# Optimization experiments

Hardware: AMD Instinct MI355X
Metric: run time of the kernel (lower is better)

## Reference

```python
import jax, jax.numpy as jnp
import numpy as np

N, E, G, L, H, DIN = 50000, 800000, 500, 4, 64, 128
EPS = 1e-5


def _gcn(x, W, b, src, dst, n):
    h = x @ W
    loop = jnp.arange(n)
    s = jnp.concatenate([src, loop])
    d = jnp.concatenate([dst, loop])
    deg = jax.ops.segment_sum(jnp.ones(s.shape[0], x.dtype), d, num_segments=n)
    dinv = jax.lax.rsqrt(jnp.maximum(deg, 1.0))  # deg >= 1 due to self loops
    norm = (dinv[s] * dinv[d])[:, None]
    return jax.ops.segment_sum(h[s] * norm, d, num_segments=n) + b


def _g2(x, W, b, src, dst, n, p=2.0):
    # G2 gradient gate: tau = tanh(scatter_mean_over_src(|X_src - X_dst|^p))
    Xc = jax.nn.relu(_gcn(x, W, b, src, dst, n))
    diff = jnp.abs(Xc[src] - Xc[dst]) ** p  # [E, H]
    s = jax.ops.segment_sum(diff, src, num_segments=n)
    cnt = jax.ops.segment_sum(jnp.ones(src.shape[0], x.dtype), src, num_segments=n)
    return jnp.tanh(s / jnp.maximum(cnt, 1.0)[:, None])


def _bn(x, g, b):
    # BatchNorm1d with batch statistics (training-mode normalization)
    m = x.mean(0)
    v = x.var(0)
    return (x - m) * jax.lax.rsqrt(v + EPS) * g + b


def setup_inputs() -> dict:
    key = jax.random.key(0)
    ks = jax.random.split(key, 24)
    sc_in = 1.0 / np.sqrt(DIN)
    sc_h = 1.0 / np.sqrt(H)
    inp = {
        "x": jax.random.normal(ks[0], (N, DIN), jnp.float32),
        "edge_index": jax.random.randint(ks[1], (2, E), 0, N),
        "batch": jnp.sort(jax.random.randint(ks[2], (N,), 0, G)),
        "preW": jax.random.normal(ks[3], (DIN, H), jnp.float32) * sc_in,
        "preb": jnp.zeros((H,), jnp.float32),
        "convW": jax.random.normal(ks[4], (L, H, H), jnp.float32) * sc_h,
        "convb": jnp.zeros((L, H), jnp.float32),
        "ggW": jax.random.normal(ks[5], (L, H, H), jnp.float32) * sc_h,
        "ggb": jnp.zeros((L, H), jnp.float32),
        "lin1W": jax.random.normal(ks[6], (H, H), jnp.float32) * sc_h,
        "lin1b": jnp.zeros((H,), jnp.float32),
        "lin2W": jax.random.normal(ks[7], (H, H), jnp.float32) * sc_h,
        "lin2b": jnp.zeros((H,), jnp.float32),
        "lin3W": jax.random.normal(ks[8], (H, H), jnp.float32) * sc_h,
        "lin3b": jnp.zeros((H,), jnp.float32),
        "lin4W": jax.random.normal(ks[9], (H, 1), jnp.float32) * sc_h,
        "lin4b": jnp.zeros((1,), jnp.float32),
        "bn_g": jnp.ones((H,), jnp.float32),
        "bn_b": jnp.zeros((H,), jnp.float32),
    }
    return inp


def reference(x, edge_index, batch, preW, preb, convW, convb, ggW, ggb,
              lin1W, lin1b, lin2W, lin2b, lin3W, lin3b, lin4W, lin4b,
              bn_g, bn_b):
    src, dst = edge_index[0], edge_index[1]
    # prelinear (dropout disabled / eval)
    x = jax.nn.relu(x @ preW + preb)
    for l in range(L):
        x_ = jax.nn.relu(_gcn(x, convW[l], convb[l], src, dst, N))
        tau = _g2(x, ggW[l], ggb[l], src, dst, N)
        x = (1.0 - tau) * x + tau * x_
    # readout: global add pool per graph -> [G, H]
    h = jax.ops.segment_sum(x, batch, num_segments=G)
    out = jax.nn.relu(_bn(h @ lin1W + lin1b, bn_g, bn_b))
    out = jax.nn.relu(_bn(out @ lin2W + lin2b, bn_g, bn_b))
    out = jax.nn.relu(_bn(out @ lin3W + lin3b, bn_g, bn_b))
    out = out @ lin4W + lin4b  # [G, 1]
    energy = 0.5 * jnp.sum((x[src] - x[dst]) ** 2)  # dirichlet energy of final x
    return (out, out, energy)
```

## Files before the change

kernel.cpp:

```cpp
#include <hip/hip_runtime.h>
#include <hip/hip_bf16.h>


#define N_NODES 50000
#define N_EDGES 800000
#define N_GRAPH 500
#define N_LAYERS 4
#define HDIM 64
#define DDIN 128
#define BN_EPS 1e-5f
#define NEPART 256
#define SC_CHUNK 2048
#define SC_NBLK ((N_NODES + SC_CHUNK - 1) / SC_CHUNK)
#define NPARTS 8
#define PRNG (N_NODES / NPARTS)
#define FILL_BPP 56

typedef __hip_bfloat16 bf16;


__global__ __launch_bounds__(256) void k_degrees(const int* __restrict__ ei,
                                                 int* __restrict__ deg_in,
                                                 int* __restrict__ deg_out) {
  int part = blockIdx.x & (NPARTS - 1);
  int slice = blockIdx.x >> 3;
  int nslice = gridDim.x >> 3;
  int lo = part * PRNG, hi = lo + PRNG;
  int stride = nslice * 256;
  for (int e = slice * 256 + threadIdx.x; e < N_EDGES; e += stride) {
    int s = ei[e], d = ei[N_EDGES + e];
    if (s >= lo && s < hi) atomicAdd(&deg_out[s], 1);
    if (d >= lo && d < hi) atomicAdd(&deg_in[d], 1);
  }
}

__global__ __launch_bounds__(256) void k_scan1(const int* __restrict__ deg_in,
                                               const int* __restrict__ deg_out,
                                               int* __restrict__ rp_dst,
                                               int* __restrict__ rp_src,
                                               int* __restrict__ bsum) {
  int arr = blockIdx.y;
  const int* in = arr ? deg_out : deg_in;
  int* out = arr ? rp_src : rp_dst;
  int base = blockIdx.x * SC_CHUNK + threadIdx.x * 8;
  int v[8];
  int s = 0;
#pragma unroll
  for (int j = 0; j < 8; ++j) {
    int ii = base + j;
    v[j] = (ii < N_NODES) ? in[ii] : 0;
    s += v[j];
  }
  __shared__ int sh[256];
  sh[threadIdx.x] = s;
  __syncthreads();
  for (int off = 1; off < 256; off <<= 1) {
    int t = (threadIdx.x >= off) ? sh[threadIdx.x - off] : 0;
    __syncthreads();
    sh[threadIdx.x] += t;
    __syncthreads();
  }
  int run = sh[threadIdx.x] - s;
#pragma unroll
  for (int j = 0; j < 8; ++j) {
    int ii = base + j;
    if (ii < N_NODES) out[ii] = run;
    run += v[j];
  }
  if (threadIdx.x == 255) bsum[arr * SC_NBLK + blockIdx.x] = sh[255];
}

__global__ __launch_bounds__(64) void k_scan2(const int* __restrict__ bsum,
                                              int* __restrict__ boff,
                                              int* __restrict__ rp_dst,
                                              int* __restrict__ rp_src) {
  int lane = threadIdx.x;
  for (int a = 0; a < 2; ++a) {
    int v = (lane < SC_NBLK) ? bsum[a * SC_NBLK + lane] : 0;
    int incl = v;
    for (int off = 1; off < 64; off <<= 1) {
      int t = __shfl_up(incl, off);
      if (lane >= off) incl += t;
    }
    if (lane < SC_NBLK) boff[a * SC_NBLK + lane] = incl - v;
  }
  if (lane == 0) {
    rp_dst[N_NODES] = N_EDGES;
    rp_src[N_NODES] = N_EDGES;
  }
}

__global__ __launch_bounds__(256) void k_scan3(const int* __restrict__ boff,
                                               int* __restrict__ rp_dst,
                                               int* __restrict__ rp_src,
                                               int* __restrict__ cur_dst,
                                               int* __restrict__ cur_src,
                                               const int* __restrict__ deg_in,
                                               float* __restrict__ dinv) {
  int arr = blockIdx.y;
  int* rp = arr ? rp_src : rp_dst;
  int* cur = arr ? cur_src : cur_dst;
  int off = boff[arr * SC_NBLK + blockIdx.x];
  int base = blockIdx.x * SC_CHUNK + threadIdx.x * 8;
#pragma unroll
  for (int j = 0; j < 8; ++j) {
    int ii = base + j;
    if (ii < N_NODES) {
      int v = rp[ii] + off;
      rp[ii] = v;
      cur[ii] = v;
      if (arr == 0) dinv[ii] = rsqrtf((float)(deg_in[ii] + 1));
    }
  }
}

__global__ __launch_bounds__(256) void k_fill(const int* __restrict__ ei,
                                              int* __restrict__ cur_dst,
                                              int* __restrict__ cur_src,
                                              int* __restrict__ csr_dst,
                                              int* __restrict__ csr_src) {
  int part = blockIdx.x & (NPARTS - 1);
  int slice = blockIdx.x >> 3;
  int nslice = gridDim.x >> 3;
  int lo = part * PRNG, hi = lo + PRNG;
  int stride = nslice * 256;
  for (int e = slice * 256 + threadIdx.x; e < N_EDGES; e += stride) {
    int s = ei[e], d = ei[N_EDGES + e];
    if (d >= lo && d < hi) {
      int q = atomicAdd(&cur_dst[d], 1);
      csr_dst[q] = s;
    }
    if (s >= lo && s < hi) {
      int q = atomicAdd(&cur_src[s], 1);
      csr_src[q] = d;
    }
  }
}


__global__ __launch_bounds__(256) void k_prelin(const float* __restrict__ x0,
                                                const float* __restrict__ W,
                                                const float* __restrict__ b,
                                                const float* __restrict__ dinv,
                                                float* __restrict__ x,
                                                float* __restrict__ xs) {
  __shared__ float Ws[DDIN * HDIM];
  for (int t = threadIdx.x; t < DDIN * HDIM; t += 256) Ws[t] = W[t];
  __syncthreads();
  int wave = threadIdx.x >> 6, lane = threadIdx.x & 63;
  float bias = b[lane];
  int stride = gridDim.x * 4;
  for (int i = blockIdx.x * 4 + wave; i < N_NODES; i += stride) {
    const float* xr = x0 + (size_t)i * DDIN;
    float xl0 = xr[lane], xl1 = xr[64 + lane];
    float acc = bias;
#pragma unroll
    for (int k = 0; k < 64; ++k) acc = fmaf(__shfl(xl0, k), Ws[k * 64 + lane], acc);
#pragma unroll
    for (int k = 0; k < 64; ++k) acc = fmaf(__shfl(xl1, k), Ws[(64 + k) * 64 + lane], acc);
    float xv = fmaxf(acc, 0.f);
    size_t li = (size_t)i * HDIM + lane;
    x[li] = xv;
    xs[li] = xv * dinv[i];
  }
}

__global__ __launch_bounds__(256) void k_agg(const float* __restrict__ xs,
                                             const int* __restrict__ rp,
                                             const int* __restrict__ csr,
                                             const float* __restrict__ dinv,
                                             float* __restrict__ aggb) {
  int i = (blockIdx.x * 256 + threadIdx.x) >> 6;
  int lane = threadIdx.x & 63;
  if (i >= N_NODES) return;
  int e0 = rp[i], e1 = rp[i + 1];
  float di = dinv[i];
  size_t li = (size_t)i * HDIM + lane;
  float a0 = xs[li], a1 = 0.f, a2 = 0.f, a3 = 0.f;
  for (int base = e0; base < e1; base += 64) {
    int m = e1 - base;
    if (m > 64) m = 64;
    int idx = csr[base + (lane < m ? lane : 0)];
    int k = 0;
    for (; k + 8 <= m; k += 8) {
      int s0 = __shfl(idx, k), s1 = __shfl(idx, k + 1), s2 = __shfl(idx, k + 2),
          s3 = __shfl(idx, k + 3), s4 = __shfl(idx, k + 4), s5 = __shfl(idx, k + 5),
          s6 = __shfl(idx, k + 6), s7 = __shfl(idx, k + 7);
      float v0 = xs[(size_t)s0 * HDIM + lane], v1 = xs[(size_t)s1 * HDIM + lane];
      float v2 = xs[(size_t)s2 * HDIM + lane], v3 = xs[(size_t)s3 * HDIM + lane];
      float v4 = xs[(size_t)s4 * HDIM + lane], v5 = xs[(size_t)s5 * HDIM + lane];
      float v6 = xs[(size_t)s6 * HDIM + lane], v7 = xs[(size_t)s7 * HDIM + lane];
      a0 += v0;
      a1 += v1;
      a2 += v2;
      a3 += v3;
      a0 += v4;
      a1 += v5;
      a2 += v6;
      a3 += v7;
    }
    for (; k < m; ++k) {
      int s = __shfl(idx, k);
      a0 += xs[(size_t)s * HDIM + lane];
    }
  }
  aggb[li] = (a0 + a1 + a2 + a3) * di;
}

__global__ __launch_bounds__(256) void k_gemm2(const float* __restrict__ agg,
                                               const float* __restrict__ W1,
                                               const float* __restrict__ W2,
                                               const float* __restrict__ b1,
                                               const float* __restrict__ b2,
                                               float* __restrict__ x_,
                                               bf16* __restrict__ Xch) {
  __shared__ float W1s[HDIM * HDIM], W2s[HDIM * HDIM];
  for (int t = threadIdx.x; t < HDIM * HDIM; t += 256) {
    W1s[t] = W1[t];
    W2s[t] = W2[t];
  }
  __syncthreads();
  int wave = threadIdx.x >> 6, lane = threadIdx.x & 63;
  float bb1 = b1[lane], bb2 = b2[lane];
  int stride = gridDim.x * 4;
  for (int i = blockIdx.x * 4 + wave; i < N_NODES; i += stride) {
    size_t li = (size_t)i * HDIM + lane;
    float xl = agg[li];
    float r1 = 0.f, r2 = 0.f;
#pragma unroll
    for (int k = 0; k < 64; ++k) {
      float xv = __shfl(xl, k);
      r1 = fmaf(xv, W1s[k * 64 + lane], r1);
      r2 = fmaf(xv, W2s[k * 64 + lane], r2);
    }
    x_[li] = fmaxf(r1 + bb1, 0.f);
    Xch[li] = __float2bfloat16(fmaxf(r2 + bb2, 0.f));
  }
}

__global__ __launch_bounds__(256) void k_gate(const bf16* __restrict__ Xch,
                                              const float* __restrict__ x_,
                                              const int* __restrict__ rp,
                                              const int* __restrict__ csr,
                                              const float* __restrict__ dinv,
                                              float* __restrict__ x,
                                              bf16* __restrict__ xh,
                                              float* __restrict__ xs) {
  int i = (blockIdx.x * 256 + threadIdx.x) >> 6;
  int lane = threadIdx.x & 63;
  if (i >= N_NODES) return;
  int e0 = rp[i], e1 = rp[i + 1];
  float xi = __bfloat162float(Xch[(size_t)i * HDIM + lane]);
  float a0 = 0.f, a1 = 0.f, a2 = 0.f, a3 = 0.f;
  for (int base = e0; base < e1; base += 64) {
    int m = e1 - base;
    if (m > 64) m = 64;
    int idx = csr[base + (lane < m ? lane : 0)];
    int k = 0;
    for (; k + 8 <= m; k += 8) {
      int s0 = __shfl(idx, k), s1 = __shfl(idx, k + 1), s2 = __shfl(idx, k + 2),
          s3 = __shfl(idx, k + 3), s4 = __shfl(idx, k + 4), s5 = __shfl(idx, k + 5),
          s6 = __shfl(idx, k + 6), s7 = __shfl(idx, k + 7);
      float v0 = __bfloat162float(Xch[(size_t)s0 * HDIM + lane]);
      float v1 = __bfloat162float(Xch[(size_t)s1 * HDIM + lane]);
      float v2 = __bfloat162float(Xch[(size_t)s2 * HDIM + lane]);
      float v3 = __bfloat162float(Xch[(size_t)s3 * HDIM + lane]);
      float v4 = __bfloat162float(Xch[(size_t)s4 * HDIM + lane]);
      float v5 = __bfloat162float(Xch[(size_t)s5 * HDIM + lane]);
      float v6 = __bfloat162float(Xch[(size_t)s6 * HDIM + lane]);
      float v7 = __bfloat162float(Xch[(size_t)s7 * HDIM + lane]);
      float t0 = xi - v0, t1 = xi - v1, t2 = xi - v2, t3 = xi - v3;
      float t4 = xi - v4, t5 = xi - v5, t6 = xi - v6, t7 = xi - v7;
      a0 = fmaf(t0, t0, a0);
      a1 = fmaf(t1, t1, a1);
      a2 = fmaf(t2, t2, a2);
      a3 = fmaf(t3, t3, a3);
      a0 = fmaf(t4, t4, a0);
      a1 = fmaf(t5, t5, a1);
      a2 = fmaf(t6, t6, a2);
      a3 = fmaf(t7, t7, a3);
    }
    for (; k < m; ++k) {
      int d = __shfl(idx, k);
      float t = xi - __bfloat162float(Xch[(size_t)d * HDIM + lane]);
      a0 = fmaf(t, t, a0);
    }
  }
  int cnt = e1 - e0;
  float tau = tanhf((a0 + a1 + a2 + a3) / (float)(cnt > 0 ? cnt : 1));
  size_t idx = (size_t)i * HDIM + lane;
  float xn = (1.f - tau) * x[idx] + tau * x_[idx];
  x[idx] = xn;
  xh[idx] = __float2bfloat16(xn);
  xs[idx] = xn * dinv[i];
}

__global__ __launch_bounds__(256) void k_epool(const bf16* __restrict__ xh,
                                               const int* __restrict__ rp,
                                               const int* __restrict__ csr,
                                               float* __restrict__ epart) {
  int i = (blockIdx.x * 256 + threadIdx.x) >> 6;
  int lane = threadIdx.x & 63;
  if (i >= N_NODES) return;
  size_t li = (size_t)i * HDIM + lane;
  float xi = __bfloat162float(xh[li]);
  int e0 = rp[i], e1 = rp[i + 1];
  float a0 = 0.f, a1 = 0.f, a2 = 0.f, a3 = 0.f;
  for (int base = e0; base < e1; base += 64) {
    int m = e1 - base;
    if (m > 64) m = 64;
    int idx = csr[base + (lane < m ? lane : 0)];
    int k = 0;
    for (; k + 8 <= m; k += 8) {
      int s0 = __shfl(idx, k), s1 = __shfl(idx, k + 1), s2 = __shfl(idx, k + 2),
          s3 = __shfl(idx, k + 3), s4 = __shfl(idx, k + 4), s5 = __shfl(idx, k + 5),
          s6 = __shfl(idx, k + 6), s7 = __shfl(idx, k + 7);
      float v0 = __bfloat162float(xh[(size_t)s0 * HDIM + lane]);
      float v1 = __bfloat162float(xh[(size_t)s1 * HDIM + lane]);
      float v2 = __bfloat162float(xh[(size_t)s2 * HDIM + lane]);
      float v3 = __bfloat162float(xh[(size_t)s3 * HDIM + lane]);
      float v4 = __bfloat162float(xh[(size_t)s4 * HDIM + lane]);
      float v5 = __bfloat162float(xh[(size_t)s5 * HDIM + lane]);
      float v6 = __bfloat162float(xh[(size_t)s6 * HDIM + lane]);
      float v7 = __bfloat162float(xh[(size_t)s7 * HDIM + lane]);
      float t0 = xi - v0, t1 = xi - v1, t2 = xi - v2, t3 = xi - v3;
      float t4 = xi - v4, t5 = xi - v5, t6 = xi - v6, t7 = xi - v7;
      a0 = fmaf(t0, t0, a0);
      a1 = fmaf(t1, t1, a1);
      a2 = fmaf(t2, t2, a2);
      a3 = fmaf(t3, t3, a3);
      a0 = fmaf(t4, t4, a0);
      a1 = fmaf(t5, t5, a1);
      a2 = fmaf(t6, t6, a2);
      a3 = fmaf(t7, t7, a3);
    }
    for (; k < m; ++k) {
      int d = __shfl(idx, k);
      float t = xi - __bfloat162float(xh[(size_t)d * HDIM + lane]);
      a0 = fmaf(t, t, a0);
    }
  }
  float acc = a0 + a1 + a2 + a3;
  acc += __shfl_down(acc, 32);
  acc += __shfl_down(acc, 16);
  acc += __shfl_down(acc, 8);
  acc += __shfl_down(acc, 4);
  acc += __shfl_down(acc, 2);
  acc += __shfl_down(acc, 1);
  if (lane == 0) atomicAdd(&epart[i & (NEPART - 1)], acc);
}

__global__ __launch_bounds__(256) void k_esum(const float* __restrict__ epart,
                                              float* __restrict__ out_e) {
  __shared__ float sh[NEPART];
  int t = threadIdx.x;
  sh[t] = epart[t];
  __syncthreads();
  for (int off = NEPART / 2; off > 0; off >>= 1) {
    if (t < off) sh[t] += sh[t + off];
    __syncthreads();
  }
  if (t == 0) out_e[0] = 0.5f * sh[0];
}

__global__ __launch_bounds__(256) void k_pool2(const float* __restrict__ x,
                                               const int* __restrict__ batch,
                                               float* __restrict__ hpool) {
  int g = blockIdx.x;
  int a = 0, b = N_NODES;
  while (a < b) {
    int mid = (a + b) >> 1;
    if (batch[mid] < g) a = mid + 1; else b = mid;
  }
  int lo = a;
  b = N_NODES;
  while (a < b) {
    int mid = (a + b) >> 1;
    if (batch[mid] < g + 1) a = mid + 1; else b = mid;
  }
  int hi = a;
  int wave = threadIdx.x >> 6, lane = threadIdx.x & 63;
  float acc = 0.f;
  for (int i = lo + wave; i < hi; i += 4) acc += x[(size_t)i * HDIM + lane];
  __shared__ float sh[4][HDIM];
  sh[wave][lane] = acc;
  __syncthreads();
  if (wave == 0)
    hpool[g * HDIM + lane] = (sh[0][lane] + sh[1][lane]) + (sh[2][lane] + sh[3][lane]);
}


__global__ __launch_bounds__(256) void k_mlpbn(const float* __restrict__ Hin,
                                               const float* __restrict__ W,
                                               const float* __restrict__ b,
                                               const float* __restrict__ g,
                                               const float* __restrict__ bb,
                                               float* __restrict__ Z) {
  int c = blockIdx.x;
  __shared__ float Wc[HDIM];
  __shared__ float red[256];
  if (threadIdx.x < HDIM) Wc[threadIdx.x] = W[threadIdx.x * HDIM + c];
  __syncthreads();
  int r0 = threadIdx.x, r1 = threadIdx.x + 256;
  float bc = b[c];
  float d0 = bc, d1 = bc;
  if (r0 < N_GRAPH) {
    const float* h = Hin + (size_t)r0 * HDIM;
#pragma unroll
    for (int k = 0; k < HDIM; ++k) d0 = fmaf(h[k], Wc[k], d0);
  }
  if (r1 < N_GRAPH) {
    const float* h = Hin + (size_t)r1 * HDIM;
#pragma unroll
    for (int k = 0; k < HDIM; ++k) d1 = fmaf(h[k], Wc[k], d1);
  }
  red[threadIdx.x] = (r0 < N_GRAPH ? d0 : 0.f) + (r1 < N_GRAPH ? d1 : 0.f);
  __syncthreads();
  for (int off = 128; off > 0; off >>= 1) {
    if (threadIdx.x < off) red[threadIdx.x] += red[threadIdx.x + off];
    __syncthreads();
  }
  float mean = red[0] / (float)N_GRAPH;
  __syncthreads();
  float t0 = (r0 < N_GRAPH) ? d0 - mean : 0.f;
  float t1 = (r1 < N_GRAPH) ? d1 - mean : 0.f;
  red[threadIdx.x] = t0 * t0 + t1 * t1;
  __syncthreads();
  for (int off = 128; off > 0; off >>= 1) {
    if (threadIdx.x < off) red[threadIdx.x] += red[threadIdx.x + off];
    __syncthreads();
  }
  float var = red[0] / (float)N_GRAPH;
  float scale = rsqrtf(var + BN_EPS) * g[c];
  float bias = bb[c];
  if (r0 < N_GRAPH) Z[(size_t)r0 * HDIM + c] = fmaxf(fmaf(t0, scale, bias), 0.f);
  if (r1 < N_GRAPH) Z[(size_t)r1 * HDIM + c] = fmaxf(fmaf(t1, scale, bias), 0.f);
}

__global__ __launch_bounds__(256) void k_final(const float* __restrict__ H,
                                               const float* __restrict__ w,
                                               const float* __restrict__ b,
                                               float* __restrict__ out) {
  int r = blockIdx.x * 256 + threadIdx.x;
  if (r >= N_GRAPH) return;
  float acc = b[0];
#pragma unroll
  for (int k = 0; k < 64; ++k) acc = fmaf(H[r * HDIM + k], w[k], acc);
  out[r] = acc;
  out[N_GRAPH + r] = acc;
}


extern "C" void kernel_launch(void* const* d_in, const int* in_sizes, int n_in,
                              void* d_out, int out_size, void* d_ws, size_t ws_size,
                              hipStream_t stream) {
  (void)in_sizes; (void)n_in; (void)out_size; (void)ws_size;
  const float* x0    = (const float*)d_in[0];
  const int*   ei    = (const int*)d_in[1];
  const int*   batch = (const int*)d_in[2];
  const float* preW  = (const float*)d_in[3];
  const float* preb  = (const float*)d_in[4];
  const float* convW = (const float*)d_in[5];
  const float* convb = (const float*)d_in[6];
  const float* ggW   = (const float*)d_in[7];
  const float* ggb   = (const float*)d_in[8];
  const float* lin1W = (const float*)d_in[9];
  const float* lin1b = (const float*)d_in[10];
  const float* lin2W = (const float*)d_in[11];
  const float* lin2b = (const float*)d_in[12];
  const float* lin3W = (const float*)d_in[13];
  const float* lin3b = (const float*)d_in[14];
  const float* lin4W = (const float*)d_in[15];
  const float* lin4b = (const float*)d_in[16];
  const float* bng   = (const float*)d_in[17];
  const float* bnb   = (const float*)d_in[18];
  float* out = (float*)d_out;

  char* ws = (char*)d_ws;
  size_t off = 0;
  auto alloc = [&](size_t bytes) -> void* {
    off = (off + 255) & ~(size_t)255;
    void* p = ws + off;
    off += bytes;
    return p;
  };
  int* deg_in   = (int*)alloc(2ull * N_NODES * 4);
  int* deg_out  = deg_in + N_NODES;
  int* rp_dst   = (int*)alloc((N_NODES + 1) * 4);
  int* rp_src   = (int*)alloc((N_NODES + 1) * 4);
  int* cur_dst  = (int*)alloc((N_NODES + 1) * 4);
  int* cur_src  = (int*)alloc((N_NODES + 1) * 4);
  int* bsum     = (int*)alloc(2 * SC_NBLK * 4);
  int* boff     = (int*)alloc(2 * SC_NBLK * 4);
  int* csr_dst  = (int*)alloc((size_t)N_EDGES * 4);
  int* csr_src  = (int*)alloc((size_t)N_EDGES * 4);
  float* dinv   = (float*)alloc(N_NODES * 4);
  float* x      = (float*)alloc((size_t)N_NODES * HDIM * 4);
  float* xs     = (float*)alloc((size_t)N_NODES * HDIM * 4);
  float* aggb   = (float*)alloc((size_t)N_NODES * HDIM * 4);
  float* x_     = (float*)alloc((size_t)N_NODES * HDIM * 4);
  bf16* Xch     = (bf16*)alloc((size_t)N_NODES * HDIM * 2);
  bf16* xh      = (bf16*)alloc((size_t)N_NODES * HDIM * 2);
  float* hpool  = (float*)alloc(N_GRAPH * HDIM * 4);
  float* epart  = (float*)alloc(NEPART * 4);
  float* mlpA   = (float*)alloc(N_GRAPH * HDIM * 4);
  float* mlpB   = (float*)alloc(N_GRAPH * HDIM * 4);

  hipMemsetAsync(deg_in, 0, 2ull * N_NODES * 4, stream);
  hipMemsetAsync(epart, 0, NEPART * 4, stream);

  k_degrees<<<NPARTS * FILL_BPP, 256, 0, stream>>>(ei, deg_in, deg_out);
  {
    dim3 g(SC_NBLK, 2);
    k_scan1<<<g, 256, 0, stream>>>(deg_in, deg_out, rp_dst, rp_src, bsum);
    k_scan2<<<1, 64, 0, stream>>>(bsum, boff, rp_dst, rp_src);
    k_scan3<<<g, 256, 0, stream>>>(boff, rp_dst, rp_src, cur_dst, cur_src, deg_in, dinv);
  }
  k_fill<<<NPARTS * FILL_BPP, 256, 0, stream>>>(ei, cur_dst, cur_src, csr_dst, csr_src);

  k_prelin<<<512, 256, 0, stream>>>(x0, preW, preb, dinv, x, xs);

  const int gnode = (N_NODES + 3) / 4;
  for (int l = 0; l < N_LAYERS; ++l) {
    k_agg<<<gnode, 256, 0, stream>>>(xs, rp_dst, csr_dst, dinv, aggb);
    k_gemm2<<<1024, 256, 0, stream>>>(aggb, convW + l * HDIM * HDIM, ggW + l * HDIM * HDIM,
                                      convb + l * HDIM, ggb + l * HDIM, x_, Xch);
    k_gate<<<gnode, 256, 0, stream>>>(Xch, x_, rp_src, csr_src, dinv, x, xh, xs);
  }

  k_epool<<<gnode, 256, 0, stream>>>(xh, rp_src, csr_src, epart);
  k_esum<<<1, NEPART, 0, stream>>>(epart, out + 2 * N_GRAPH);
  k_pool2<<<N_GRAPH, 256, 0, stream>>>(x, batch, hpool);

  k_mlpbn<<<HDIM, 256, 0, stream>>>(hpool, lin1W, lin1b, bng, bnb, mlpA);
  k_mlpbn<<<HDIM, 256, 0, stream>>>(mlpA, lin2W, lin2b, bng, bnb, mlpB);
  k_mlpbn<<<HDIM, 256, 0, stream>>>(mlpB, lin3W, lin3b, bng, bnb, mlpA);
  k_final<<<(N_GRAPH + 255) / 256, 256, 0, stream>>>(mlpA, lin4W, lin4b, out);
}
```

Measured before the change: 879.4 us.

## Split waves into half-waves gathering two neighbors per step with vector loads

The aggregation, gate and energy gather kernels now assign each half-wave to a different neighbor row. Each lane loads two features at once, as a float2 or as a packed bf16 pair, so a wave fetches two neighbor rows per instruction, and the half-wave partials are combined with a cross-half shuffle at the end. Edge-index and CSR reads are switched to nontemporal loads. This widens per-lane memory transactions and halves the number of gather instructions. In exchange, the final store runs on only half the lanes and a shuffle reduction is added.

```diff
diff --git a/kernel.cpp b/kernel.cpp
--- a/kernel.cpp
+++ b/kernel.cpp
@@ -18,6 +18,17 @@
 
 typedef __hip_bfloat16 bf16;
 
+__device__ __forceinline__ float bflo(unsigned int u) {
+  return __uint_as_float(u << 16);
+}
+__device__ __forceinline__ float bfhi(unsigned int u) {
+  return __uint_as_float(u & 0xffff0000u);
+}
+__device__ __forceinline__ unsigned short f2bf(float f) {
+  bf16 h = __float2bfloat16(f);
+  return *reinterpret_cast<unsigned short*>(&h);
+}
+
 
 __global__ __launch_bounds__(256) void k_degrees(const int* __restrict__ ei,
                                                  int* __restrict__ deg_in,
@@ -28,7 +39,8 @@
   int lo = part * PRNG, hi = lo + PRNG;
   int stride = nslice * 256;
   for (int e = slice * 256 + threadIdx.x; e < N_EDGES; e += stride) {
-    int s = ei[e], d = ei[N_EDGES + e];
+    int s = __builtin_nontemporal_load(ei + e);
+    int d = __builtin_nontemporal_load(ei + N_EDGES + e);
     if (s >= lo && s < hi) atomicAdd(&deg_out[s], 1);
     if (d >= lo && d < hi) atomicAdd(&deg_in[d], 1);
   }
@@ -125,7 +137,8 @@
   int lo = part * PRNG, hi = lo + PRNG;
   int stride = nslice * 256;
   for (int e = slice * 256 + threadIdx.x; e < N_EDGES; e += stride) {
-    int s = ei[e], d = ei[N_EDGES + e];
+    int s = __builtin_nontemporal_load(ei + e);
+    int d = __builtin_nontemporal_load(ei + N_EDGES + e);
     if (d >= lo && d < hi) {
       int q = atomicAdd(&cur_dst[d], 1);
       csr_dst[q] = s;
@@ -165,6 +178,7 @@
   }
 }
 
+
 __global__ __launch_bounds__(256) void k_agg(const float* __restrict__ xs,
                                              const int* __restrict__ rp,
                                              const int* __restrict__ csr,
@@ -173,38 +187,52 @@
   int i = (blockIdx.x * 256 + threadIdx.x) >> 6;
   int lane = threadIdx.x & 63;
   if (i >= N_NODES) return;
+  int half = lane >> 5, fl = lane & 31;
+  const float2* xs2 = (const float2*)xs;
   int e0 = rp[i], e1 = rp[i + 1];
   float di = dinv[i];
-  size_t li = (size_t)i * HDIM + lane;
-  float a0 = xs[li], a1 = 0.f, a2 = 0.f, a3 = 0.f;
+  float2 a0 = make_float2(0.f, 0.f), a1 = a0, a2 = a0, a3 = a0;
+  if (half == 0) a0 = xs2[(size_t)i * 32 + fl];
   for (int base = e0; base < e1; base += 64) {
     int m = e1 - base;
     if (m > 64) m = 64;
-    int idx = csr[base + (lane < m ? lane : 0)];
+    int idx = __builtin_nontemporal_load(csr + base + (lane < m ? lane : 0));
     int k = 0;
-    for (; k + 8 <= m; k += 8) {
-      int s0 = __shfl(idx, k), s1 = __shfl(idx, k + 1), s2 = __shfl(idx, k + 2),
-          s3 = __shfl(idx, k + 3), s4 = __shfl(idx, k + 4), s5 = __shfl(idx, k + 5),
-          s6 = __shfl(idx, k + 6), s7 = __shfl(idx, k + 7);
-      float v0 = xs[(size_t)s0 * HDIM + lane], v1 = xs[(size_t)s1 * HDIM + lane];
-      float v2 = xs[(size_t)s2 * HDIM + lane], v3 = xs[(size_t)s3 * HDIM + lane];
-      float v4 = xs[(size_t)s4 * HDIM + lane], v5 = xs[(size_t)s5 * HDIM + lane];
-      float v6 = xs[(size_t)s6 * HDIM + lane], v7 = xs[(size_t)s7 * HDIM + lane];
-      a0 += v0;
-      a1 += v1;
-      a2 += v2;
-      a3 += v3;
-      a0 += v4;
-      a1 += v5;
-      a2 += v6;
-      a3 += v7;
-    }
-    for (; k < m; ++k) {
-      int s = __shfl(idx, k);
-      a0 += xs[(size_t)s * HDIM + lane];
-    }
-  }
-  aggb[li] = (a0 + a1 + a2 + a3) * di;
+    for (; k + 16 <= m; k += 16) {
+      int r0 = __shfl(idx, k + half),      r1 = __shfl(idx, k + 2 + half);
+      int r2 = __shfl(idx, k + 4 + half),  r3 = __shfl(idx, k + 6 + half);
+      int r4 = __shfl(idx, k + 8 + half),  r5 = __shfl(idx, k + 10 + half);
+      int r6 = __shfl(idx, k + 12 + half), r7 = __shfl(idx, k + 14 + half);
+      float2 v0 = xs2[(size_t)r0 * 32 + fl], v1 = xs2[(size_t)r1 * 32 + fl];
+      float2 v2 = xs2[(size_t)r2 * 32 + fl], v3 = xs2[(size_t)r3 * 32 + fl];
+      float2 v4 = xs2[(size_t)r4 * 32 + fl], v5 = xs2[(size_t)r5 * 32 + fl];
+      float2 v6 = xs2[(size_t)r6 * 32 + fl], v7 = xs2[(size_t)r7 * 32 + fl];
+      a0.x += v0.x; a0.y += v0.y; a1.x += v1.x; a1.y += v1.y;
+      a2.x += v2.x; a2.y += v2.y; a3.x += v3.x; a3.y += v3.y;
+      a0.x += v4.x; a0.y += v4.y; a1.x += v5.x; a1.y += v5.y;
+      a2.x += v6.x; a2.y += v6.y; a3.x += v7.x; a3.y += v7.y;
+    }
+    for (; k < m; k += 2) {
+      int kk = k + half;
+      int r = __shfl(idx, kk < m ? kk : k);
+      if (kk < m) {
+        float2 v = xs2[(size_t)r * 32 + fl];
+        a0.x += v.x;
+        a0.y += v.y;
+      }
+    }
+  }
+  float2 a;
+  a.x = (a0.x + a1.x) + (a2.x + a3.x);
+  a.y = (a0.y + a1.y) + (a2.y + a3.y);
+  a.x += __shfl_xor(a.x, 32);
+  a.y += __shfl_xor(a.y, 32);
+  if (half == 0) {
+    float2 r;
+    r.x = a.x * di;
+    r.y = a.y * di;
+    ((float2*)aggb)[(size_t)i * 32 + fl] = r;
+  }
 }
 
 __global__ __launch_bounds__(256) void k_gemm2(const float* __restrict__ agg,
@@ -249,50 +277,79 @@
   int i = (blockIdx.x * 256 + threadIdx.x) >> 6;
   int lane = threadIdx.x & 63;
   if (i >= N_NODES) return;
+  int half = lane >> 5, fl = lane & 31;
+  const unsigned int* X2 = (const unsigned int*)Xch;
   int e0 = rp[i], e1 = rp[i + 1];
-  float xi = __bfloat162float(Xch[(size_t)i * HDIM + lane]);
-  float a0 = 0.f, a1 = 0.f, a2 = 0.f, a3 = 0.f;
+  unsigned int xiu = X2[(size_t)i * 32 + fl];
+  float xiA = bflo(xiu), xiB = bfhi(xiu);
+  float sA0 = 0.f, sA1 = 0.f, sB0 = 0.f, sB1 = 0.f;
   for (int base = e0; base < e1; base += 64) {
     int m = e1 - base;
     if (m > 64) m = 64;
-    int idx = csr[base + (lane < m ? lane : 0)];
+    int idx = __builtin_nontemporal_load(csr + base + (lane < m ? lane : 0));
     int k = 0;
-    for (; k + 8 <= m; k += 8) {
-      int s0 = __shfl(idx, k), s1 = __shfl(idx, k + 1), s2 = __shfl(idx, k + 2),
-          s3 = __shfl(idx, k + 3), s4 = __shfl(idx, k + 4), s5 = __shfl(idx, k + 5),
-          s6 = __shfl(idx, k + 6), s7 = __shfl(idx, k + 7);
-      float v0 = __bfloat162float(Xch[(size_t)s0 * HDIM + lane]);
-      float v1 = __bfloat162float(Xch[(size_t)s1 * HDIM + lane]);
-      float v2 = __bfloat162float(Xch[(size_t)s2 * HDIM + lane]);
-      float v3 = __bfloat162float(Xch[(size_t)s3 * HDIM + lane]);
-      float v4 = __bfloat162float(Xch[(size_t)s4 * HDIM + lane]);
-      float v5 = __bfloat162float(Xch[(size_t)s5 * HDIM + lane]);
-      float v6 = __bfloat162float(Xch[(size_t)s6 * HDIM + lane]);
-      float v7 = __bfloat162float(Xch[(size_t)s7 * HDIM + lane]);
-      float t0 = xi - v0, t1 = xi - v1, t2 = xi - v2, t3 = xi - v3;
-      float t4 = xi - v4, t5 = xi - v5, t6 = xi - v6, t7 = xi - v7;
-      a0 = fmaf(t0, t0, a0);
-      a1 = fmaf(t1, t1, a1);
-      a2 = fmaf(t2, t2, a2);
-      a3 = fmaf(t3, t3, a3);
-      a0 = fmaf(t4, t4, a0);
-      a1 = fmaf(t5, t5, a1);
-      a2 = fmaf(t6, t6, a2);
-      a3 = fmaf(t7, t7, a3);
-    }
-    for (; k < m; ++k) {
-      int d = __shfl(idx, k);
-      float t = xi - __bfloat162float(Xch[(size_t)d * HDIM + lane]);
-      a0 = fmaf(t, t, a0);
-    }
-  }
+    for (; k + 16 <= m; k += 16) {
+      int r0 = __shfl(idx, k + half),      r1 = __shfl(idx, k + 2 + half);
+      int r2 = __shfl(idx, k + 4 + half),  r3 = __shfl(idx, k + 6 + half);
+      int r4 = __shfl(idx, k + 8 + half),  r5 = __shfl(idx, k + 10 + half);
+      int r6 = __shfl(idx, k + 12 + half), r7 = __shfl(idx, k + 14 + half);
+      unsigned int u0 = X2[(size_t)r0 * 32 + fl], u1 = X2[(size_t)r1 * 32 + fl];
+      unsigned int u2 = X2[(size_t)r2 * 32 + fl], u3 = X2[(size_t)r3 * 32 + fl];
+      unsigned int u4 = X2[(size_t)r4 * 32 + fl], u5 = X2[(size_t)r5 * 32 + fl];
+      unsigned int u6 = X2[(size_t)r6 * 32 + fl], u7 = X2[(size_t)r7 * 32 + fl];
+      float t;
+      t = xiA - bflo(u0); sA0 = fmaf(t, t, sA0);
+      t = xiB - bfhi(u0); sB0 = fmaf(t, t, sB0);
+      t = xiA - bflo(u1); sA1 = fmaf(t, t, sA1);
+      t = xiB - bfhi(u1); sB1 = fmaf(t, t, sB1);
+      t = xiA - bflo(u2); sA0 = fmaf(t, t, sA0);
+      t = xiB - bfhi(u2); sB0 = fmaf(t, t, sB0);
+      t = xiA - bflo(u3); sA1 = fmaf(t, t, sA1);
+      t = xiB - bfhi(u3); sB1 = fmaf(t, t, sB1);
+      t = xiA - bflo(u4); sA0 = fmaf(t, t, sA0);
+      t = xiB - bfhi(u4); sB0 = fmaf(t, t, sB0);
+      t = xiA - bflo(u5); sA1 = fmaf(t, t, sA1);
+      t = xiB - bfhi(u5); sB1 = fmaf(t, t, sB1);
+      t = xiA - bflo(u6); sA0 = fmaf(t, t, sA0);
+      t = xiB - bfhi(u6); sB0 = fmaf(t, t, sB0);
+      t = xiA - bflo(u7); sA1 = fmaf(t, t, sA1);
+      t = xiB - bfhi(u7); sB1 = fmaf(t, t, sB1);
+    }
+    for (; k < m; k += 2) {
+      int kk = k + half;
+      int r = __shfl(idx, kk < m ? kk : k);
+      if (kk < m) {
+        unsigned int u = X2[(size_t)r * 32 + fl];
+        float t = xiA - bflo(u);
+        sA0 = fmaf(t, t, sA0);
+        t = xiB - bfhi(u);
+        sB0 = fmaf(t, t, sB0);
+      }
+    }
+  }
+  float sA = sA0 + sA1, sB = sB0 + sB1;
+  sA += __shfl_xor(sA, 32);
+  sB += __shfl_xor(sB, 32);
   int cnt = e1 - e0;
-  float tau = tanhf((a0 + a1 + a2 + a3) / (float)(cnt > 0 ? cnt : 1));
-  size_t idx = (size_t)i * HDIM + lane;
-  float xn = (1.f - tau) * x[idx] + tau * x_[idx];
-  x[idx] = xn;
-  xh[idx] = __float2bfloat16(xn);
-  xs[idx] = xn * dinv[i];
+  float inv = 1.f / (float)(cnt > 0 ? cnt : 1);
+  float tauA = tanhf(sA * inv);
+  float tauB = tanhf(sB * inv);
+  if (half == 0) {
+    float di = dinv[i];
+    size_t o = (size_t)i * 32 + fl;
+    float2 xv = ((const float2*)x)[o];
+    float2 xn_ = ((const float2*)x_)[o];
+    float2 xn;
+    xn.x = (1.f - tauA) * xv.x + tauA * xn_.x;
+    xn.y = (1.f - tauB) * xv.y + tauB * xn_.y;
+    ((float2*)x)[o] = xn;
+    float2 xsv;
+    xsv.x = xn.x * di;
+    xsv.y = xn.y * di;
+    ((float2*)xs)[o] = xsv;
+    ((unsigned int*)xh)[o] =
+        (unsigned int)f2bf(xn.x) | ((unsigned int)f2bf(xn.y) << 16);
+  }
 }
 
 __global__ __launch_bounds__(256) void k_epool(const bf16* __restrict__ xh,
@@ -302,45 +359,57 @@
   int i = (blockIdx.x * 256 + threadIdx.x) >> 6;
   int lane = threadIdx.x & 63;
   if (i >= N_NODES) return;
-  size_t li = (size_t)i * HDIM + lane;
-  float xi = __bfloat162float(xh[li]);
+  int half = lane >> 5, fl = lane & 31;
+  const unsigned int* X2 = (const unsigned int*)xh;
+  unsigned int xiu = X2[(size_t)i * 32 + fl];
+  float xiA = bflo(xiu), xiB = bfhi(xiu);
   int e0 = rp[i], e1 = rp[i + 1];
   float a0 = 0.f, a1 = 0.f, a2 = 0.f, a3 = 0.f;
   for (int base = e0; base < e1; base += 64) {
     int m = e1 - base;
     if (m > 64) m = 64;
-    int idx = csr[base + (lane < m ? lane : 0)];
+    int idx = __builtin_nontemporal_load(csr + base + (lane < m ? lane : 0));
     int k = 0;
-    for (; k + 8 <= m; k += 8) {
-      int s0 = __shfl(idx, k), s1 = __shfl(idx, k + 1), s2 = __shfl(idx, k + 2),
-          s3 = __shfl(idx, k + 3), s4 = __shfl(idx, k + 4), s5 = __shfl(idx, k + 5),
-          s6 = __shfl(idx, k + 6), s7 = __shfl(idx, k + 7);
-      float v0 = __bfloat162float(xh[(size_t)s0 * HDIM + lane]);
-      float v1 = __bfloat162float(xh[(size_t)s1 * HDIM + lane]);
-      float v2 = __bfloat162float(xh[(size_t)s2 * HDIM + lane]);
-      float v3 = __bfloat162float(xh[(size_t)s3 * HDIM + lane]);
-      float v4 = __bfloat162float(xh[(size_t)s4 * HDIM + lane]);
-      float v5 = __bfloat162float(xh[(size_t)s5 * HDIM + lane]);
-      float v6 = __bfloat162float(xh[(size_t)s6 * HDIM + lane]);
-      float v7 = __bfloat162float(xh[(size_t)s7 * HDIM + lane]);
-      float t0 = xi - v0, t1 = xi - v1, t2 = xi - v2, t3 = xi - v3;
-      float t4 = xi - v4, t5 = xi - v5, t6 = xi - v6, t7 = xi - v7;
-      a0 = fmaf(t0, t0, a0);
-      a1 = fmaf(t1, t1, a1);
-      a2 = fmaf(t2, t2, a2);
-      a3 = fmaf(t3, t3, a3);
-      a0 = fmaf(t4, t4, a0);
-      a1 = fmaf(t5, t5, a1);
-      a2 = fmaf(t6, t6, a2);
-      a3 = fmaf(t7, t7, a3);
-    }
-    for (; k < m; ++k) {
-      int d = __shfl(idx, k);
-      float t = xi - __bfloat162float(xh[(size_t)d * HDIM + lane]);
-      a0 = fmaf(t, t, a0);
-    }
-  }
-  float acc = a0 + a1 + a2 + a3;
+    for (; k + 16 <= m; k += 16) {
+      int r0 = __shfl(idx, k + half),      r1 = __shfl(idx, k + 2 + half);
+      int r2 = __shfl(idx, k + 4 + half),  r3 = __shfl(idx, k + 6 + half);
+      int r4 = __shfl(idx, k + 8 + half),  r5 = __shfl(idx, k + 10 + half);
+      int r6 = __shfl(idx, k + 12 + half), r7 = __shfl(idx, k + 14 + half);
+      unsigned int u0 = X2[(size_t)r0 * 32 + fl], u1 = X2[(size_t)r1 * 32 + fl];
+      unsigned int u2 = X2[(size_t)r2 * 32 + fl], u3 = X2[(size_t)r3 * 32 + fl];
+      unsigned int u4 = X2[(size_t)r4 * 32 + fl], u5 = X2[(size_t)r5 * 32 + fl];
+      unsigned int u6 = X2[(size_t)r6 * 32 + fl], u7 = X2[(size_t)r7 * 32 + fl];
+      float t;
+      t = xiA - bflo(u0); a0 = fmaf(t, t, a0);
+      t = xiB - bfhi(u0); a1 = fmaf(t, t, a1);
+      t = xiA - bflo(u1); a2 = fmaf(t, t, a2);
+      t = xiB - bfhi(u1); a3 = fmaf(t, t, a3);
+      t = xiA - bflo(u2); a0 = fmaf(t, t, a0);
+      t = xiB - bfhi(u2); a1 = fmaf(t, t, a1);
+      t = xiA - bflo(u3); a2 = fmaf(t, t, a2);
+      t = xiB - bfhi(u3); a3 = fmaf(t, t, a3);
+      t = xiA - bflo(u4); a0 = fmaf(t, t, a0);
+      t = xiB - bfhi(u4); a1 = fmaf(t, t, a1);
+      t = xiA - bflo(u5); a2 = fmaf(t, t, a2);
+      t = xiB - bfhi(u5); a3 = fmaf(t, t, a3);
+      t = xiA - bflo(u6); a0 = fmaf(t, t, a0);
+      t = xiB - bfhi(u6); a1 = fmaf(t, t, a1);
+      t = xiA - bflo(u7); a2 = fmaf(t, t, a2);
+      t = xiB - bfhi(u7); a3 = fmaf(t, t, a3);
+    }
+    for (; k < m; k += 2) {
+      int kk = k + half;
+      int r = __shfl(idx, kk < m ? kk : k);
+      if (kk < m) {
+        unsigned int u = X2[(size_t)r * 32 + fl];
+        float t = xiA - bflo(u);
+        a0 = fmaf(t, t, a0);
+        t = xiB - bfhi(u);
+        a1 = fmaf(t, t, a1);
+      }
+    }
+  }
+  float acc = (a0 + a1) + (a2 + a3);
   acc += __shfl_down(acc, 32);
   acc += __shfl_down(acc, 16);
   acc += __shfl_down(acc, 8);
```

Result: slower. 921.1 us (+4.7%).
